# Performance work log

Measured on AMD Instinct MI355X. Metric: run time of the kernel, lower is better.

The kernel has to match this reference:

```python
import jax, jax.numpy as jnp
import numpy as np

E = 100          # number of elements
K = 4            # codes per element (core set = all elements)
C = E * K        # total codes
D = 128          # embed_dim
N = 262144       # atoms in batch
GAMMA = 0.99     # ema_decay
BETA = 0.25      # commitment_weight


def setup_inputs() -> dict:
    key = jax.random.key(0)
    k1, k2, k3, k4 = jax.random.split(key, 4)
    h = jax.random.normal(k1, (N, D), dtype=jnp.float32)
    elem_indices = jax.random.randint(k2, (N,), 0, E, dtype=jnp.int32)
    codebook = jax.random.normal(k3, (C, D), dtype=jnp.float32)
    ema_count = jax.random.uniform(k4, (C,), dtype=jnp.float32, minval=0.5, maxval=2.0)
    ema_embed_sum = codebook * ema_count[:, None]
    return {"h": h, "elem_indices": elem_indices, "codebook": codebook,
            "ema_count": ema_count, "ema_embed_sum": ema_embed_sum}


def reference(h, elem_indices, codebook, ema_count, ema_embed_sum):
    # element id owning each code (uniform contiguous ranges of size K)
    code_elem = jnp.repeat(jnp.arange(E, dtype=elem_indices.dtype), K)  # [C]

    # masked cdist (euclidean): ||h||^2 + ||c||^2 - 2 h.c, inf outside own range
    d2 = (jnp.sum(h * h, axis=1, keepdims=True)
          + jnp.sum(codebook * codebook, axis=1)[None, :]
          - 2.0 * h @ codebook.T)                                # [N, C]
    dist = jnp.sqrt(jnp.maximum(d2, 0.0))
    valid = jnp.where(code_elem[None, :] == elem_indices[:, None], dist, jnp.inf)

    atom_types = jnp.argmin(valid, axis=1)                       # [N]
    z_q = codebook[atom_types]                                   # [N, D]
    h_q = h + jax.lax.stop_gradient(z_q - h)                     # straight-through

    # all elements are multi-code -> commitment over every atom
    commitment_loss = jnp.mean((h - jax.lax.stop_gradient(z_q)) ** 2)
    vq_loss = BETA * commitment_loss

    # EMA codebook update (training path, no_grad in original)
    counts = jax.ops.segment_sum(jnp.ones((N,), h.dtype), atom_types, num_segments=C)  # [C]
    sums = jax.ops.segment_sum(h, atom_types, num_segments=C)                          # [C, D]
    elem_present = jax.ops.segment_sum(jnp.ones((N,), h.dtype), elem_indices,
                                       num_segments=E) > 0                              # [E]
    code_present = jnp.repeat(elem_present, K)                                          # [C]

    new_count = jnp.where(code_present, GAMMA * ema_count + (1.0 - GAMMA) * counts, ema_count)
    new_sum = jnp.where(code_present[:, None],
                        GAMMA * ema_embed_sum + (1.0 - GAMMA) * sums, ema_embed_sum)
    new_codebook = jnp.where(code_present[:, None],
                             new_sum / jnp.maximum(new_count, 1e-5)[:, None], codebook)

    return h_q, atom_types, vq_loss, new_codebook, new_count, new_sum
```

## Files before the change

kernel.cpp:

```cpp
#include <hip/hip_runtime.h>
#include <hip/hip_bf16.h>

#define D_ 128
#define E_ 100
#define K_ 4
#define C_ 400
#define NCHUNK 128
#define SCALE 65536.0f
#define INV_SCALE (1.0f / 65536.0f)

#define OFF_COUNTS 51200
#define OFF_LOSS   51600
#define OFF_PSUM   51712
#define PSUM_SZ    (256 * C_ * 64)
#define OFF_PCNT   (OFF_PSUM + PSUM_SZ)
#define WS_NEED_PART ((size_t)(OFF_PCNT + NCHUNK * C_) * 4)

template <int CTRL>
__device__ __forceinline__ float dpp_add(float x) {
  int y = __builtin_amdgcn_update_dpp(0, __builtin_bit_cast(int, x),
                                      CTRL, 0xF, 0xF, true);
  return x + __builtin_bit_cast(float, y);
}

__device__ __forceinline__ float dist8(float4 hA, float4 hB, float4 cA, float4 cB) {
  float d0 = hA.x - cA.x, d1 = hA.y - cA.y;
  float d2 = hA.z - cA.z, d3 = hA.w - cA.w;
  float d4 = hB.x - cB.x, d5 = hB.y - cB.y;
  float d6 = hB.z - cB.z, d7 = hB.w - cB.w;
  return ((d0*d0 + d1*d1) + (d2*d2 + d3*d3)) +
         ((d4*d4 + d5*d5) + (d6*d6 + d7*d7));
}

__global__ __launch_bounds__(1024) void k_asg(
    const float* __restrict__ h, const int* __restrict__ ei,
    const float* __restrict__ cb, float* __restrict__ hq,
    float* __restrict__ at, float* __restrict__ loss_acc,
    int N, int elo, int ehi) {
  __shared__ float4 cbl[200 * 33];
  __shared__ float wl[16];
  const int tid = threadIdx.x;
  const float4* cb4 = (const float4*)cb;
  const int nrow = (ehi - elo) * K_;
  for (int idx = tid; idx < nrow * 32; idx += 1024) {
    int r = idx >> 5, k = idx & 31;
    cbl[r * 33 + k] = cb4[(size_t)(elo * K_ + r) * 32 + k];
  }
  __syncthreads();

  const int t = tid & 15;
  const int gid = blockIdx.x * 64 + (tid >> 4);
  const int ngroups = gridDim.x * 64;
  const float4* h4 = (const float4*)h;
  float4* hq4 = (float4*)hq;
  float loss = 0.f;

  int e = ei[gid < N ? gid : 0];
  for (int a = gid; a < N; a += ngroups) {
    const int an = a + ngroups;
    const int en = ei[an < N ? an : a];
    if (e >= elo && e < ehi) {
      float4 hA = h4[(size_t)a * 32 + t * 2];
      float4 hB = h4[(size_t)a * 32 + t * 2 + 1];
      const int r0 = (e - elo) * K_;
      float4 cA0 = cbl[(r0+0)*33 + t*2], cB0 = cbl[(r0+0)*33 + t*2 + 1];
      float4 cA1 = cbl[(r0+1)*33 + t*2], cB1 = cbl[(r0+1)*33 + t*2 + 1];
      float4 cA2 = cbl[(r0+2)*33 + t*2], cB2 = cbl[(r0+2)*33 + t*2 + 1];
      float4 cA3 = cbl[(r0+3)*33 + t*2], cB3 = cbl[(r0+3)*33 + t*2 + 1];

      float p0 = dist8(hA, hB, cA0, cB0);
      float p1 = dist8(hA, hB, cA1, cB1);
      float p2 = dist8(hA, hB, cA2, cB2);
      float p3 = dist8(hA, hB, cA3, cB3);

      p0 = dpp_add<0xB1>(p0); p1 = dpp_add<0xB1>(p1);
      p2 = dpp_add<0xB1>(p2); p3 = dpp_add<0xB1>(p3);
      p0 = dpp_add<0x4E>(p0); p1 = dpp_add<0x4E>(p1);
      p2 = dpp_add<0x4E>(p2); p3 = dpp_add<0x4E>(p3);
      p0 = dpp_add<0x141>(p0); p1 = dpp_add<0x141>(p1);
      p2 = dpp_add<0x141>(p2); p3 = dpp_add<0x141>(p3);
      p0 = dpp_add<0x140>(p0); p1 = dpp_add<0x140>(p1);
      p2 = dpp_add<0x140>(p2); p3 = dpp_add<0x140>(p3);

      int best = 0; float bp = p0;
      if (p1 < bp) { bp = p1; best = 1; }
      if (p2 < bp) { bp = p2; best = 2; }
      if (p3 < bp) { bp = p3; best = 3; }

      float4 qA = cA0, qB = cB0;
      if (best == 1) { qA = cA1; qB = cB1; }
      if (best == 2) { qA = cA2; qB = cB2; }
      if (best == 3) { qA = cA3; qB = cB3; }
      hq4[(size_t)a * 32 + t * 2]     = qA;
      hq4[(size_t)a * 32 + t * 2 + 1] = qB;
      if (t == 0) {
        at[a] = (float)(e * K_ + best);
        loss += bp;
      }
    }
    e = en;
  }

  loss += __shfl_xor(loss, 16, 64);
  loss += __shfl_xor(loss, 32, 64);
  if ((tid & 63) == 0) wl[tid >> 6] = loss;
  __syncthreads();
  if (tid == 0) {
    float s = 0.f;
#pragma unroll
    for (int i = 0; i < 16; ++i) s += wl[i];
    atomicAdd(loss_acc, s);
  }
}

__global__ __launch_bounds__(1024) void k_sums3(
    const float* __restrict__ h, const float* __restrict__ at,
    int* __restrict__ psumI, int* __restrict__ pcntI,
    float* __restrict__ sums, float* __restrict__ countsF,
    int dopart, int N) {
  const int half = blockIdx.x & 1;
  const int chunk = blockIdx.x >> 1;
  __shared__ int acc[C_ * 64];
  __shared__ int cnt[C_];
  for (int i = threadIdx.x; i < C_ * 64; i += 1024) acc[i] = 0;
  if (half == 0)
    for (int i = threadIdx.x; i < C_; i += 1024) cnt[i] = 0;
  __syncthreads();

  const int per = (N + NCHUNK - 1) / NCHUNK;
  const int a0 = chunk * per;
  const int aEnd = min(a0 + per, N);
  const int w = threadIdx.x >> 6;
  const int lane = threadIdx.x & 63;
  const int g = lane >> 4, t = lane & 15;
  const float4* h4 = (const float4*)h;

  int a = a0 + w * 4 + g;
  bool ok0 = a < aEnd, ok1 = (a + 64) < aEnd;
  float4 v0 = {}, v1 = {}; int c0 = 0, c1 = 0;
  if (ok0) { v0 = h4[(size_t)a * 32 + half * 16 + t]; c0 = (int)at[a]; }
  if (ok1) { v1 = h4[(size_t)(a + 64) * 32 + half * 16 + t]; c1 = (int)at[a + 64]; }

  while (ok0) {
    const int an = a + 128;
    const bool okn = an < aEnd;
    float4 vn = {}; int cn = 0;
    if (okn) { vn = h4[(size_t)an * 32 + half * 16 + t]; cn = (int)at[an]; }

    int* ap = &acc[c0 * 64 + t * 4];
    int iv0 = __float2int_rn(v0.x * SCALE);
    int iv1 = __float2int_rn(v0.y * SCALE);
    int iv2 = __float2int_rn(v0.z * SCALE);
    int iv3 = __float2int_rn(v0.w * SCALE);
    if (g == 0) { atomicAdd(&ap[0],iv0); atomicAdd(&ap[1],iv1); atomicAdd(&ap[2],iv2); atomicAdd(&ap[3],iv3); }
    else if (g == 1) { atomicAdd(&ap[1],iv1); atomicAdd(&ap[2],iv2); atomicAdd(&ap[3],iv3); atomicAdd(&ap[0],iv0); }
    else if (g == 2) { atomicAdd(&ap[2],iv2); atomicAdd(&ap[3],iv3); atomicAdd(&ap[0],iv0); atomicAdd(&ap[1],iv1); }
    else { atomicAdd(&ap[3],iv3); atomicAdd(&ap[0],iv0); atomicAdd(&ap[1],iv1); atomicAdd(&ap[2],iv2); }
    if (half == 0 && t == 0) atomicAdd(&cnt[c0], 1);

    a += 64;
    ok0 = ok1; v0 = v1; c0 = c1;
    ok1 = okn; v1 = vn; c1 = cn;
  }
  __syncthreads();

  if (dopart) {
    int* pb = psumI + (size_t)blockIdx.x * (C_ * 64);
    for (int i = threadIdx.x; i < C_ * 64; i += 1024) pb[i] = acc[i];
    if (half == 0) {
      int* pc = pcntI + (size_t)chunk * C_;
      for (int i = threadIdx.x; i < C_; i += 1024) pc[i] = cnt[i];
    }
  } else {
    for (int i = threadIdx.x; i < C_ * 64; i += 1024) {
      int vv = acc[i];
      if (vv != 0)
        atomicAdd(&sums[(size_t)(i >> 6) * D_ + half * 64 + (i & 63)],
                  (float)vv * INV_SCALE);
    }
    if (half == 0)
      for (int i = threadIdx.x; i < C_; i += 1024)
        if (cnt[i] != 0) atomicAdd(&countsF[i], (float)cnt[i]);
  }
}

__global__ __launch_bounds__(256) void k_reduce(
    const int* __restrict__ psumI, const int* __restrict__ pcntI,
    float* __restrict__ sums, float* __restrict__ countsF) {
  int idx = blockIdx.x * 256 + threadIdx.x;
  if (idx < C_ * D_) {
    int code = idx >> 7;
    int dim = idx & 127;
    int half = dim >> 6;
    int dl = dim & 63;
    const int* p = psumI + (size_t)half * (C_ * 64) + code * 64 + dl;
    float s = 0.f;
    for (int b = 0; b < NCHUNK; ++b)
      s += (float)p[(size_t)b * 2 * (C_ * 64)];
    sums[idx] = s * INV_SCALE;
  }
  if (idx < C_) {
    int s = 0;
    for (int b = 0; b < NCHUNK; ++b)
      s += pcntI[(size_t)b * C_ + idx];
    countsF[idx] = (float)s;
  }
}

__global__ __launch_bounds__(256) void k_final(
    const float* __restrict__ cb, const float* __restrict__ ecnt,
    const float* __restrict__ esum, const float* __restrict__ ws,
    float* __restrict__ out, int N) {
  const float* sums = ws;
  const float* countsF = ws + OFF_COUNTS;
  int idx = blockIdx.x * 256 + threadIdx.x;
  const size_t base = (size_t)N * D_ + N + 1;
  if (idx < C_ * D_) {
    int c = idx >> 7;
    int e4 = (c >> 2) << 2;
    bool present = (countsF[e4] + countsF[e4 + 1] + countsF[e4 + 2] + countsF[e4 + 3]) > 0.f;
    float es = esum[idx];
    float s  = sums[idx];
    float ns = present ? 0.99f * es + 0.01f * s : es;
    float ec = ecnt[c];
    float nc = present ? 0.99f * ec + 0.01f * countsF[c] : ec;
    float ncbv = present ? ns / fmaxf(nc, 1e-5f) : cb[idx];
    out[base + idx] = ncbv;
    if ((idx & 127) == 0) out[base + C_ * D_ + c] = nc;
    out[base + C_ * D_ + C_ + idx] = ns;
  }
  if (idx == 0) {
    float loss = ws[OFF_LOSS];
    out[(size_t)N * D_ + N] = 0.25f * loss / ((float)N * (float)D_);
  }
}

extern "C" void kernel_launch(void* const* d_in, const int* in_sizes, int n_in,
                              void* d_out, int out_size, void* d_ws, size_t ws_size,
                              hipStream_t stream) {
  const float* h = nullptr; const int* ei = nullptr;
  const float* cb = nullptr; const float* ecnt = nullptr; const float* esum = nullptr;
  long hsz = -1; int hidx = -1;
  for (int i = 0; i < n_in; ++i)
    if ((long)in_sizes[i] > hsz) { hsz = in_sizes[i]; hidx = i; }
  h = (const float*)d_in[hidx];
  const int N = (int)(hsz / D_);
  for (int i = 0; i < n_in; ++i) {
    if (i == hidx) continue;
    const int s = in_sizes[i];
    if (s == N) ei = (const int*)d_in[i];
    else if (s == C_) ecnt = (const float*)d_in[i];
    else if (s == C_ * D_) { if (!cb) cb = (const float*)d_in[i]; else esum = (const float*)d_in[i]; }
  }

  float* out = (float*)d_out;
  float* hq  = out;
  float* at  = out + (size_t)N * D_;

  float* ws = (float*)d_ws;
  float* sums    = ws;
  float* countsF = ws + OFF_COUNTS;
  float* lossp   = ws + OFF_LOSS;
  int*   psumI   = (int*)(ws + OFF_PSUM);
  int*   pcntI   = (int*)(ws + OFF_PCNT);

  const int dopart = (ws_size >= WS_NEED_PART) ? 1 : 0;

  hipMemsetAsync(d_ws, 0, (size_t)(OFF_LOSS + 1) * 4, stream);

  k_asg<<<256, 1024, 0, stream>>>(h, ei, cb, hq, at, lossp, N, 0, E_ / 2);
  k_asg<<<256, 1024, 0, stream>>>(h, ei, cb, hq, at, lossp, N, E_ / 2, E_);
  k_sums3<<<NCHUNK * 2, 1024, 0, stream>>>(h, at, psumI, pcntI,
                                           sums, countsF, dopart, N);
  if (dopart)
    k_reduce<<<(C_ * D_ + 255) / 256, 256, 0, stream>>>(psumI, pcntI, sums, countsF);
  k_final<<<(C_ * D_ + 255) / 256, 256, 0, stream>>>(cb, ecnt, esum, ws, out, N);
}
```

Measured before the change: 116.9 us.

## Replace per-atom assignment with fp16 MFMA distance over full codebook

Replaces the two per-element-range assignment kernels with one kernel that stores the whole codebook as fp16 in swizzled LDS. It computes h·c for all 400 codes with 16x16x32 MFMA tiles, then adds precomputed norms. The argmin uses packed float/index keys masked to each atom's own element range, and h_q is gathered from the fp16 codebook. This trades exact fp32 per-code distances and fp32 z_q output for dense matrix-core throughput, but does roughly 100x more multiply work. It also risks precision mismatches: fp16 codebook values in h_q, quantized norms, and truncated distance bits that change tie-breaking and the loss.

```diff
diff --git a/kernel.cpp b/kernel.cpp
--- a/kernel.cpp
+++ b/kernel.cpp
@@ -5,9 +5,12 @@
 #define E_ 100
 #define K_ 4
 #define C_ 400
+#define MB 256
 #define NCHUNK 128
 #define SCALE 65536.0f
 #define INV_SCALE (1.0f / 65536.0f)
+#define CNSCALE 4096.0f
+#define INV_CNSCALE (1.0f / 4096.0f)
 
 #define OFF_COUNTS 51200
 #define OFF_LOSS   51600
@@ -16,94 +19,122 @@
 #define OFF_PCNT   (OFF_PSUM + PSUM_SZ)
 #define WS_NEED_PART ((size_t)(OFF_PCNT + NCHUNK * C_) * 4)
 
+typedef _Float16 f16x8 __attribute__((ext_vector_type(8)));
+typedef float f32x4v __attribute__((ext_vector_type(4)));
+
 template <int CTRL>
-__device__ __forceinline__ float dpp_add(float x) {
-  int y = __builtin_amdgcn_update_dpp(0, __builtin_bit_cast(int, x),
-                                      CTRL, 0xF, 0xF, true);
-  return x + __builtin_bit_cast(float, y);
-}
-
-__device__ __forceinline__ float dist8(float4 hA, float4 hB, float4 cA, float4 cB) {
-  float d0 = hA.x - cA.x, d1 = hA.y - cA.y;
-  float d2 = hA.z - cA.z, d3 = hA.w - cA.w;
-  float d4 = hB.x - cB.x, d5 = hB.y - cB.y;
-  float d6 = hB.z - cB.z, d7 = hB.w - cB.w;
-  return ((d0*d0 + d1*d1) + (d2*d2 + d3*d3)) +
-         ((d4*d4 + d5*d5) + (d6*d6 + d7*d7));
-}
-
-__global__ __launch_bounds__(1024) void k_asg(
+__device__ __forceinline__ unsigned dpp_minu(unsigned x) {
+  unsigned y = (unsigned)__builtin_amdgcn_update_dpp(0, (int)x, CTRL, 0xF, 0xF, true);
+  return x < y ? x : y;
+}
+
+__global__ __launch_bounds__(1024) void k_dist(
     const float* __restrict__ h, const int* __restrict__ ei,
     const float* __restrict__ cb, float* __restrict__ hq,
-    float* __restrict__ at, float* __restrict__ loss_acc,
-    int N, int elo, int ehi) {
-  __shared__ float4 cbl[200 * 33];
+    float* __restrict__ at, float* __restrict__ loss_acc, int N) {
+  __shared__ __align__(16) unsigned cbls[C_ * 64];
+  __shared__ int cnormI[C_];
   __shared__ float wl[16];
   const int tid = threadIdx.x;
-  const float4* cb4 = (const float4*)cb;
-  const int nrow = (ehi - elo) * K_;
-  for (int idx = tid; idx < nrow * 32; idx += 1024) {
-    int r = idx >> 5, k = idx & 31;
-    cbl[r * 33 + k] = cb4[(size_t)(elo * K_ + r) * 32 + k];
-  }
-  __syncthreads();
-
-  const int t = tid & 15;
-  const int gid = blockIdx.x * 64 + (tid >> 4);
-  const int ngroups = gridDim.x * 64;
+
+  if (tid < C_) cnormI[tid] = 0;
+  __syncthreads();
+  {
+    const float4* cb4 = (const float4*)cb;
+    for (int idx = tid; idx < C_ * 32; idx += 1024) {
+      int code = idx >> 5, kq = idx & 31;
+      float4 f = cb4[code * 32 + kq];
+      unsigned short q0 = __builtin_bit_cast(unsigned short, (_Float16)f.x);
+      unsigned short q1 = __builtin_bit_cast(unsigned short, (_Float16)f.y);
+      unsigned short q2 = __builtin_bit_cast(unsigned short, (_Float16)f.z);
+      unsigned short q3 = __builtin_bit_cast(unsigned short, (_Float16)f.w);
+      int i = (code * 64 + kq * 2) ^ ((code & 7) << 2);
+      cbls[i]     = (unsigned)q0 | ((unsigned)q1 << 16);
+      cbls[i + 1] = (unsigned)q2 | ((unsigned)q3 << 16);
+      float sq = f.x * f.x + f.y * f.y + f.z * f.z + f.w * f.w;
+      atomicAdd(&cnormI[code], __float2int_rn(sq * CNSCALE));
+    }
+  }
+  __syncthreads();
+
+  const int w = tid >> 6, l = tid & 63;
+  const int row = l & 15, g = l >> 4;
+  const int abase = blockIdx.x * MB + w * 16;
   const float4* h4 = (const float4*)h;
+
+  const int aload = min(abase + row, N - 1);
+  int e = ei[aload];
+  float hn = 0.f;
+  f16x8 af0, af1, af2, af3;
+#define LOADA(K, AF) { \
+    float4 u = h4[(size_t)aload * 32 + (K) * 8 + g * 2]; \
+    float4 v = h4[(size_t)aload * 32 + (K) * 8 + g * 2 + 1]; \
+    AF[0]=(_Float16)u.x; AF[1]=(_Float16)u.y; AF[2]=(_Float16)u.z; AF[3]=(_Float16)u.w; \
+    AF[4]=(_Float16)v.x; AF[5]=(_Float16)v.y; AF[6]=(_Float16)v.z; AF[7]=(_Float16)v.w; \
+    hn += u.x*u.x + u.y*u.y + u.z*u.z + u.w*u.w \
+        + v.x*v.x + v.y*v.y + v.z*v.z + v.w*v.w; }
+  LOADA(0, af0) LOADA(1, af1) LOADA(2, af2) LOADA(3, af3)
+#undef LOADA
+  hn += __shfl_xor(hn, 16, 64);
+  hn += __shfl_xor(hn, 32, 64);
+  const int ec0 = 4 * __shfl(e, g * 4 + 0, 64), ec1 = 4 * __shfl(e, g * 4 + 1, 64),
+            ec2 = 4 * __shfl(e, g * 4 + 2, 64), ec3 = 4 * __shfl(e, g * 4 + 3, 64);
+  const float hn0 = __shfl(hn, g * 4 + 0, 64), hn1 = __shfl(hn, g * 4 + 1, 64),
+              hn2 = __shfl(hn, g * 4 + 2, 64), hn3 = __shfl(hn, g * 4 + 3, 64);
+
+  const unsigned sx = (unsigned)((row & 7) << 2);
+  unsigned b0 = 0x7F800000u, b1 = 0x7F800000u, b2 = 0x7F800000u, b3 = 0x7F800000u;
+  for (int t = 0; t < 25; ++t) {
+    const int c = t * 16 + row;
+    const int ib = c * 64 + g * 4;
+    f32x4v acc = {0.f, 0.f, 0.f, 0.f};
+    uint4 r0 = *(const uint4*)&cbls[(unsigned)ib ^ sx];
+    acc = __builtin_amdgcn_mfma_f32_16x16x32_f16(af0, __builtin_bit_cast(f16x8, r0), acc, 0, 0, 0);
+    uint4 r1 = *(const uint4*)&cbls[(unsigned)(ib + 16) ^ sx];
+    acc = __builtin_amdgcn_mfma_f32_16x16x32_f16(af1, __builtin_bit_cast(f16x8, r1), acc, 0, 0, 0);
+    uint4 r2 = *(const uint4*)&cbls[(unsigned)(ib + 32) ^ sx];
+    acc = __builtin_amdgcn_mfma_f32_16x16x32_f16(af2, __builtin_bit_cast(f16x8, r2), acc, 0, 0, 0);
+    uint4 r3 = *(const uint4*)&cbls[(unsigned)(ib + 48) ^ sx];
+    acc = __builtin_amdgcn_mfma_f32_16x16x32_f16(af3, __builtin_bit_cast(f16x8, r3), acc, 0, 0, 0);
+    const float cnf = (float)cnormI[c] * INV_CNSCALE;
+#define STEP(J, BJ, ECJ, HNJ) { \
+    float d = fmaxf(HNJ - 2.f * acc[J] + cnf, 0.f); \
+    unsigned key = (__builtin_bit_cast(unsigned, d) & 0xFFFFFE00u) | (unsigned)c; \
+    key = ((unsigned)(c - (ECJ)) < 4u) ? key : 0x7F800000u; \
+    BJ = BJ < key ? BJ : key; }
+    STEP(0, b0, ec0, hn0) STEP(1, b1, ec1, hn1)
+    STEP(2, b2, ec2, hn2) STEP(3, b3, ec3, hn3)
+#undef STEP
+  }
+  b0 = dpp_minu<0xB1>(b0); b0 = dpp_minu<0x4E>(b0); b0 = dpp_minu<0x141>(b0); b0 = dpp_minu<0x140>(b0);
+  b1 = dpp_minu<0xB1>(b1); b1 = dpp_minu<0x4E>(b1); b1 = dpp_minu<0x141>(b1); b1 = dpp_minu<0x140>(b1);
+  b2 = dpp_minu<0xB1>(b2); b2 = dpp_minu<0x4E>(b2); b2 = dpp_minu<0x141>(b2); b2 = dpp_minu<0x140>(b2);
+  b3 = dpp_minu<0xB1>(b3); b3 = dpp_minu<0x4E>(b3); b3 = dpp_minu<0x141>(b3); b3 = dpp_minu<0x140>(b3);
+
   float4* hq4 = (float4*)hq;
   float loss = 0.f;
-
-  int e = ei[gid < N ? gid : 0];
-  for (int a = gid; a < N; a += ngroups) {
-    const int an = a + ngroups;
-    const int en = ei[an < N ? an : a];
-    if (e >= elo && e < ehi) {
-      float4 hA = h4[(size_t)a * 32 + t * 2];
-      float4 hB = h4[(size_t)a * 32 + t * 2 + 1];
-      const int r0 = (e - elo) * K_;
-      float4 cA0 = cbl[(r0+0)*33 + t*2], cB0 = cbl[(r0+0)*33 + t*2 + 1];
-      float4 cA1 = cbl[(r0+1)*33 + t*2], cB1 = cbl[(r0+1)*33 + t*2 + 1];
-      float4 cA2 = cbl[(r0+2)*33 + t*2], cB2 = cbl[(r0+2)*33 + t*2 + 1];
-      float4 cA3 = cbl[(r0+3)*33 + t*2], cB3 = cbl[(r0+3)*33 + t*2 + 1];
-
-      float p0 = dist8(hA, hB, cA0, cB0);
-      float p1 = dist8(hA, hB, cA1, cB1);
-      float p2 = dist8(hA, hB, cA2, cB2);
-      float p3 = dist8(hA, hB, cA3, cB3);
-
-      p0 = dpp_add<0xB1>(p0); p1 = dpp_add<0xB1>(p1);
-      p2 = dpp_add<0xB1>(p2); p3 = dpp_add<0xB1>(p3);
-      p0 = dpp_add<0x4E>(p0); p1 = dpp_add<0x4E>(p1);
-      p2 = dpp_add<0x4E>(p2); p3 = dpp_add<0x4E>(p3);
-      p0 = dpp_add<0x141>(p0); p1 = dpp_add<0x141>(p1);
-      p2 = dpp_add<0x141>(p2); p3 = dpp_add<0x141>(p3);
-      p0 = dpp_add<0x140>(p0); p1 = dpp_add<0x140>(p1);
-      p2 = dpp_add<0x140>(p2); p3 = dpp_add<0x140>(p3);
-
-      int best = 0; float bp = p0;
-      if (p1 < bp) { bp = p1; best = 1; }
-      if (p2 < bp) { bp = p2; best = 2; }
-      if (p3 < bp) { bp = p3; best = 3; }
-
-      float4 qA = cA0, qB = cB0;
-      if (best == 1) { qA = cA1; qB = cB1; }
-      if (best == 2) { qA = cA2; qB = cB2; }
-      if (best == 3) { qA = cA3; qB = cB3; }
-      hq4[(size_t)a * 32 + t * 2]     = qA;
-      hq4[(size_t)a * 32 + t * 2 + 1] = qB;
-      if (t == 0) {
-        at[a] = (float)(e * K_ + best);
-        loss += bp;
-      }
-    }
-    e = en;
-  }
+#define OUTJ(J, BJ) { \
+    const int colj = (int)((BJ) & 0x1FFu); \
+    const int rloc = g * 4 + (J); \
+    if (abase + rloc < N) { \
+      const size_t arow = (size_t)(abase + rloc); \
+      const unsigned swj = (unsigned)((colj & 7) << 2); \
+      uint4 raw = *(const uint4*)&cbls[(unsigned)(colj * 64 + row * 4) ^ swj]; \
+      f16x8 cv = __builtin_bit_cast(f16x8, raw); \
+      float4 o1 = make_float4((float)cv[0], (float)cv[1], (float)cv[2], (float)cv[3]); \
+      float4 o2 = make_float4((float)cv[4], (float)cv[5], (float)cv[6], (float)cv[7]); \
+      hq4[arow * 32 + row * 2]     = o1; \
+      hq4[arow * 32 + row * 2 + 1] = o2; \
+      if (row == 0) { \
+        at[arow] = (float)colj; \
+        loss += __builtin_bit_cast(float, (BJ) & 0xFFFFFE00u); \
+      } } }
+  OUTJ(0, b0) OUTJ(1, b1) OUTJ(2, b2) OUTJ(3, b3)
+#undef OUTJ
 
   loss += __shfl_xor(loss, 16, 64);
   loss += __shfl_xor(loss, 32, 64);
-  if ((tid & 63) == 0) wl[tid >> 6] = loss;
+  if (l == 0) wl[w] = loss;
   __syncthreads();
   if (tid == 0) {
     float s = 0.f;
@@ -268,8 +299,8 @@
 
   hipMemsetAsync(d_ws, 0, (size_t)(OFF_LOSS + 1) * 4, stream);
 
-  k_asg<<<256, 1024, 0, stream>>>(h, ei, cb, hq, at, lossp, N, 0, E_ / 2);
-  k_asg<<<256, 1024, 0, stream>>>(h, ei, cb, hq, at, lossp, N, E_ / 2, E_);
+  const int nblk = (N + MB - 1) / MB;
+  k_dist<<<nblk, 1024, 0, stream>>>(h, ei, cb, hq, at, lossp, N);
   k_sums3<<<NCHUNK * 2, 1024, 0, stream>>>(h, at, psumI, pcntI,
                                            sums, countsF, dopart, N);
   if (dopart)
```

New measurement: 169.5 us. 1.45x slower.
